# Kernel tuning notes

Hardware: AMD Instinct MI355X
Metric: run time of the kernel (lower is better)

Reference implementation:

```python
import jax, jax.numpy as jnp
import numpy as np
import math

B, L, D = 4, 4096, 1024
D_EMB, D_HID = 3, 16


def make_pos_emb(emb_dim, seq_len):
    # Complex exponential positional embeddings (non-trainable), shape (1, seq_len, emb_dim)
    t = np.linspace(0.0, 1.0, seq_len, dtype=np.float32)[None, :, None]
    bands = (emb_dim - 1) // 2
    t_res = np.linspace(0.0, seq_len - 1, seq_len, dtype=np.float32)[None, :, None]
    w = 2.0 * math.pi * t_res / seq_len
    f = np.linspace(0.0001, max(bands - 1, 0), bands, dtype=np.float32)[None, None]
    z = np.exp(-1j * (f * w).astype(np.complex64))
    z = np.concatenate([t, z.real.astype(np.float32), z.imag.astype(np.float32)], axis=-1)
    return jnp.asarray(z)


def setup_inputs() -> dict:
    key = jax.random.key(0)
    ks = jax.random.split(key, 8)
    u = jax.random.normal(ks[0], (B, L, D), dtype=jnp.float32)
    z = make_pos_emb(D_EMB, L)  # (1, L, D_EMB)
    # filter MLP: Linear(d_emb, d_hidden) -> ReLU -> Linear(d_hidden, d_model)
    s1 = 1.0 / math.sqrt(D_EMB)
    w1 = jax.random.uniform(ks[1], (D_HID, D_EMB), jnp.float32, -s1, s1)
    b1 = jax.random.uniform(ks[2], (D_HID,), jnp.float32, -s1, s1)
    s2 = 1.0 / math.sqrt(D_HID)
    w2 = jax.random.uniform(ks[3], (D, D_HID), jnp.float32, -s2, s2)
    b2 = jax.random.uniform(ks[4], (D,), jnp.float32, -s2, s2)
    # projection: Linear(d_model, d_model)
    sp = 1.0 / math.sqrt(D)
    pw = jax.random.uniform(ks[5], (D, D), jnp.float32, -sp, sp)
    pb = jax.random.uniform(ks[6], (D,), jnp.float32, -sp, sp)
    return {"u": u, "z": z, "w1": w1, "b1": b1, "w2": w2, "b2": b2, "pw": pw, "pb": pb}


def fft_conv(u_bdl, k_dl):
    # u_bdl: (B, D, L), k_dl: (1, D, L) or (D, L)
    seqlen = u_bdl.shape[-1]
    fft_size = 2 * seqlen
    k_f = jnp.fft.rfft(k_dl, n=fft_size) / fft_size
    u_f = jnp.fft.rfft(u_bdl, n=fft_size)
    y = jnp.fft.irfft(u_f * k_f, n=fft_size, norm="forward")[..., :seqlen]
    return y


def reference(u, z, w1, b1, w2, b2, pw, pb):
    seqlen = u.shape[1]
    pe = z[:, :seqlen]  # (1, L, D_EMB)
    h = jax.nn.relu(jnp.einsum("ble,he->blh", pe, w1) + b1)
    filt = jnp.einsum("blh,dh->bld", h, w2) + b2  # (1, L, D)
    filt = jnp.transpose(filt, (0, 2, 1))  # (1, D, L)
    u_conv = fft_conv(jnp.transpose(u, (0, 2, 1)), filt)  # (B, D, L)
    u_conv = jnp.transpose(u_conv, (0, 2, 1)).astype(u.dtype)  # (B, L, D)
    u_proj = jnp.einsum("bld,od->blo", u, pw) + pb
    return u_conv * u_proj + u
```

## Files before the change

### kernel.cpp

```cpp
#include <hip/hip_runtime.h>
#include <hip/hip_bf16.h>

#define SEQL 4096
#define DCH  1024
#define BATCH 4
#define NC   4096
#define KH   4097

typedef float2 cf;
__device__ __forceinline__ cf mkc(float x, float y){ return make_float2(x,y); }
__device__ __forceinline__ cf cadd(cf a, cf b){ return mkc(a.x+b.x, a.y+b.y); }
__device__ __forceinline__ cf csub(cf a, cf b){ return mkc(a.x-b.x, a.y-b.y); }
__device__ __forceinline__ cf cmul(cf a, cf b){ return mkc(a.x*b.x - a.y*b.y, a.x*b.y + a.y*b.x); }
__device__ __forceinline__ cf cconjf(cf a){ return mkc(a.x, -a.y); }
__device__ __forceinline__ cf addi(cf a, cf b){ return mkc(a.x - b.y, a.y + b.x); }
__device__ __forceinline__ cf subi(cf a, cf b){ return mkc(a.x + b.y, a.y - b.x); }
__device__ __forceinline__ int cpad(int i){ return i + (i >> 4); }
__device__ __forceinline__ int drev(int i){
    return ((i>>10)&3) | (((i>>8)&3)<<2) | (((i>>6)&3)<<4)
         | (((i>>4)&3)<<6) | (((i>>2)&3)<<8) | ((i&3)<<10);
}

__device__ __forceinline__ cf W1c(int j){
    const float cs[4] = {1.f, 0.92387953f, 0.70710678f, 0.38268343f};
    const float sn[4] = {0.f, -0.38268343f, -0.70710678f, -0.92387953f};
    return mkc(cs[j], sn[j]);
}
__device__ __forceinline__ cf W2c(int j){
    const float cs[4] = {1.f, 0.70710678f, 0.f, -0.70710678f};
    const float sn[4] = {0.f, -0.70710678f, -1.f, -0.70710678f};
    return mkc(cs[j], sn[j]);
}
__device__ __forceinline__ cf W3c(int j){
    const float cs[4] = {1.f, 0.38268343f, -0.70710678f, -0.92387953f};
    const float sn[4] = {0.f, -0.92387953f, -0.70710678f, 0.38268343f};
    return mkc(cs[j], sn[j]);
}

__global__ __launch_bounds__(256) void twiddle_init(cf* __restrict__ tw4, cf* __restrict__ tw8){
    int i = blockIdx.x*256 + threadIdx.x;
    const double TWO_PI = 6.283185307179586476925286766559;
    double a4 = -TWO_PI * (double)i / 4096.0;
    double a8 = -TWO_PI * (double)i / 8192.0;
    tw4[i] = mkc((float)cos(a4), (float)sin(a4));
    tw8[i] = mkc((float)cos(a8), (float)sin(a8));
}

__device__ void fft_dif(cf* lds, const cf* __restrict__ tw){
    const int tid = threadIdx.x;
#pragma unroll
    for (int p = 0; p < 4; ++p) {
        const int lm = 10 - 2*p;
        const int m  = 1 << lm;
        const int step = 1024 >> lm;
#pragma unroll
        for (int it = 0; it < 4; ++it) {
            int j = tid + (it << 8);
            int k = j & (m-1);
            int g = j >> lm;
            int i0 = (g << (lm+2)) + k;
            cf x0 = lds[cpad(i0)];
            cf x1 = lds[cpad(i0+m)];
            cf x2 = lds[cpad(i0+2*m)];
            cf x3 = lds[cpad(i0+3*m)];
            cf b0 = cadd(x0,x2), b1 = csub(x0,x2);
            cf b2 = cadd(x1,x3), b3 = csub(x1,x3);
            cf u0 = cadd(b0,b2);
            cf u2 = csub(b0,b2);
            cf u1 = subi(b1,b3);
            cf u3 = addi(b1,b3);
            int t1 = k*step;
            lds[cpad(i0)]     = u0;
            lds[cpad(i0+m)]   = cmul(u1, tw[t1]);
            lds[cpad(i0+2*m)] = cmul(u2, tw[2*t1]);
            lds[cpad(i0+3*m)] = cmul(u3, tw[3*t1]);
        }
        __syncthreads();
    }
    {
        int base = 17*tid;
        cf v[16];
#pragma unroll
        for (int j=0;j<16;++j) v[j] = lds[base+j];
#pragma unroll
        for (int j=0;j<4;++j){
            cf x0=v[j], x1=v[j+4], x2=v[j+8], x3=v[j+12];
            cf b0=cadd(x0,x2), b1=csub(x0,x2), b2=cadd(x1,x3), b3=csub(x1,x3);
            cf u0=cadd(b0,b2), u2=csub(b0,b2), u1=subi(b1,b3), u3=addi(b1,b3);
            v[j]    = u0;
            v[j+4]  = cmul(u1, W1c(j));
            v[j+8]  = cmul(u2, W2c(j));
            v[j+12] = cmul(u3, W3c(j));
        }
#pragma unroll
        for (int c=0;c<4;++c){
            cf x0=v[4*c], x1=v[4*c+1], x2=v[4*c+2], x3=v[4*c+3];
            cf b0=cadd(x0,x2), b1=csub(x0,x2), b2=cadd(x1,x3), b3=csub(x1,x3);
            v[4*c]   = cadd(b0,b2);
            v[4*c+1] = subi(b1,b3);
            v[4*c+2] = csub(b0,b2);
            v[4*c+3] = addi(b1,b3);
        }
#pragma unroll
        for (int j=0;j<16;++j) lds[base+j] = v[j];
        __syncthreads();
    }
}

__device__ void fft_dit_inv(cf* lds, const cf* __restrict__ tw){
    const int tid = threadIdx.x;
    {
        int base = 17*tid;
        cf v[16];
#pragma unroll
        for (int j=0;j<16;++j) v[j] = lds[base+j];
#pragma unroll
        for (int c=0;c<4;++c){
            cf a0=v[4*c], a1=v[4*c+1], a2=v[4*c+2], a3=v[4*c+3];
            cf b0=cadd(a0,a2), b1=csub(a0,a2), b2=cadd(a1,a3), b3=csub(a1,a3);
            v[4*c]   = cadd(b0,b2);
            v[4*c+1] = addi(b1,b3);
            v[4*c+2] = csub(b0,b2);
            v[4*c+3] = subi(b1,b3);
        }
#pragma unroll
        for (int j=0;j<4;++j){
            cf a0=v[j];
            cf a1=cmul(v[j+4],  cconjf(W1c(j)));
            cf a2=cmul(v[j+8],  cconjf(W2c(j)));
            cf a3=cmul(v[j+12], cconjf(W3c(j)));
            cf b0=cadd(a0,a2), b1=csub(a0,a2), b2=cadd(a1,a3), b3=csub(a1,a3);
            v[j]    = cadd(b0,b2);
            v[j+4]  = addi(b1,b3);
            v[j+8]  = csub(b0,b2);
            v[j+12] = subi(b1,b3);
        }
#pragma unroll
        for (int j=0;j<16;++j) lds[base+j] = v[j];
        __syncthreads();
    }
#pragma unroll
    for (int p = 0; p < 4; ++p) {
        const int lm = 4 + 2*p;
        const int m  = 1 << lm;
        const int step = 1024 >> lm;
#pragma unroll
        for (int it = 0; it < 4; ++it) {
            int j = tid + (it << 8);
            int k = j & (m-1);
            int g = j >> lm;
            int i0 = (g << (lm+2)) + k;
            int t1 = k*step;
            cf a0 = lds[cpad(i0)];
            cf a1 = cmul(lds[cpad(i0+m)],   cconjf(tw[t1]));
            cf a2 = cmul(lds[cpad(i0+2*m)], cconjf(tw[2*t1]));
            cf a3 = cmul(lds[cpad(i0+3*m)], cconjf(tw[3*t1]));
            cf b0=cadd(a0,a2), b1=csub(a0,a2), b2=cadd(a1,a3), b3=csub(a1,a3);
            lds[cpad(i0)]     = cadd(b0,b2);
            lds[cpad(i0+m)]   = addi(b1,b3);
            lds[cpad(i0+2*m)] = csub(b0,b2);
            lds[cpad(i0+3*m)] = subi(b1,b3);
        }
        __syncthreads();
    }
}

__global__ __launch_bounds__(256) void mlp_kernel(
        const float* __restrict__ z, const float* __restrict__ w1,
        const float* __restrict__ b1, float* __restrict__ h) {
    int l = blockIdx.x * blockDim.x + threadIdx.x;
    if (l >= SEQL) return;
    float pe0 = z[l * 3 + 0], pe1 = z[l * 3 + 1], pe2 = z[l * 3 + 2];
#pragma unroll
    for (int j = 0; j < 16; ++j) {
        float v = pe0 * w1[j * 3 + 0] + pe1 * w1[j * 3 + 1] + pe2 * w1[j * 3 + 2] + b1[j];
        h[l * 16 + j] = v > 0.f ? v : 0.f;
    }
}

__global__ __launch_bounds__(256) void transpose_kernel(
        const float* __restrict__ u, float* __restrict__ ut) {
    __shared__ float tile[32][33];
    int b = blockIdx.z;
    int l0 = blockIdx.x * 32;
    int d0 = blockIdx.y * 32;
    int tx = threadIdx.x, ty = threadIdx.y;
    const float* up = u + (size_t)b * SEQL * DCH;
#pragma unroll
    for (int i = 0; i < 32; i += 8)
        tile[ty + i][tx] = up[(size_t)(l0 + ty + i) * DCH + d0 + tx];
    __syncthreads();
    float* utp = ut + (size_t)b * DCH * SEQL;
#pragma unroll
    for (int i = 0; i < 32; i += 8)
        utp[(size_t)(d0 + ty + i) * SEQL + l0 + tx] = tile[tx][ty + i];
}

__global__ __launch_bounds__(256) void filt_fft_kernel(
        const float* __restrict__ h, const float* __restrict__ w2,
        const float* __restrict__ b2, const cf* __restrict__ tw4,
        const cf* __restrict__ tw8, cf* __restrict__ kf) {
    __shared__ cf lds[4352];
    int d = blockIdx.x;
    int tid = threadIdx.x;
    float w[16];
#pragma unroll
    for (int j = 0; j < 16; ++j) w[j] = w2[d * 16 + j];
    float bb = b2[d];
    for (int n = tid; n < 2048; n += 256) {
        const float* h0 = h + (size_t)(2*n) * 16;
        float f0 = bb, f1 = bb;
#pragma unroll
        for (int j = 0; j < 16; ++j) { f0 += h0[j] * w[j]; f1 += h0[16 + j] * w[j]; }
        lds[cpad(n)] = mkc(f0, f1);
    }
    for (int n = 2048 + tid; n < 4096; n += 256) lds[cpad(n)] = mkc(0.f, 0.f);
    __syncthreads();
    fft_dif(lds, tw4);
    const float s = 1.f / 8192.f;
    cf* Hrow = kf + (size_t)d * KH;
    const int lane  = tid & 63;
    const int kbase = ((lane & 31) << 6) | ((lane >> 5) << 5) | ((tid >> 6) << 3);
#pragma unroll
    for (int it = 0; it < 8; ++it) {
        int k = kbase + it;
        if (k == 0) {
            cf c0 = lds[cpad(0)];
            Hrow[0]    = mkc((c0.x + c0.y) * s, 0.f);
            Hrow[4096] = mkc((c0.x - c0.y) * s, 0.f);
            cf c2 = lds[cpad(drev(2048))];
            Hrow[2048] = mkc(c2.x * s, -c2.y * s);
        } else {
            int kk = 4096 - k;
            cf ck  = lds[cpad(drev(k))];
            cf ckk = lds[cpad(drev(kk))];
            cf cc = cconjf(ckk);
            cf E  = mkc(0.5f*(ck.x+cc.x), 0.5f*(ck.y+cc.y));
            cf Dd = csub(ck, cc);
            cf O  = mkc(0.5f*Dd.y, -0.5f*Dd.x);
            cf wv = tw8[k];
            cf Xk  = cadd(E, cmul(wv, O));
            cf wp  = mkc(-wv.x, wv.y);
            cf Xkk = cadd(cconjf(E), cmul(wp, cconjf(O)));
            Hrow[k]  = mkc(Xk.x * s, Xk.y * s);
            Hrow[kk] = mkc(Xkk.x * s, Xkk.y * s);
        }
    }
}

__global__ __launch_bounds__(256) void conv_kernel(
        float* __restrict__ uty, const cf* __restrict__ tw4,
        const cf* __restrict__ tw8, const cf* __restrict__ kf) {
    __shared__ cf lds[4352];
    int row = blockIdx.x;
    int d = row & (DCH - 1);
    int tid = threadIdx.x;
    float* rp = uty + (size_t)row * SEQL;
    for (int n = tid; n < 2048; n += 256)
        lds[cpad(n)] = *(const float2*)&rp[2*n];
    for (int n = 2048 + tid; n < 4096; n += 256) lds[cpad(n)] = mkc(0.f, 0.f);
    __syncthreads();
    fft_dif(lds, tw4);
    const cf* Hrow = kf + (size_t)d * KH;
    const int lane  = tid & 63;
    const int kbase = ((lane & 31) << 6) | ((lane >> 5) << 5) | ((tid >> 6) << 3);
#pragma unroll
    for (int it = 0; it < 8; ++it) {
        int k = kbase + it;
        if (k == 0) {
            cf c0 = lds[cpad(0)];
            float X0 = c0.x + c0.y, X4 = c0.x - c0.y;
            cf H0 = Hrow[0], H4 = Hrow[4096];
            cf Y0 = mkc(X0 * H0.x, X0 * H0.y);
            cf Y4 = mkc(X4 * H4.x, X4 * H4.y);
            cf S  = cadd(Y0, Y4), Dd = csub(Y0, Y4);
            lds[cpad(0)] = addi(S, Dd);
            int s2 = cpad(drev(2048));
            cf c2 = lds[s2];
            cf Y2 = cmul(cconjf(c2), Hrow[2048]);
            lds[s2] = mkc(2.f * Y2.x, -2.f * Y2.y);
        } else {
            int kk = 4096 - k;
            int sk = cpad(drev(k)), skk = cpad(drev(kk));
            cf ck = lds[sk], ckk = lds[skk];
            cf cc = cconjf(ckk);
            cf E  = mkc(0.5f*(ck.x+cc.x), 0.5f*(ck.y+cc.y));
            cf Dd = csub(ck, cc);
            cf O  = mkc(0.5f*Dd.y, -0.5f*Dd.x);
            cf wv = tw8[k];
            cf Xk  = cadd(E, cmul(wv, O));
            cf wp  = mkc(-wv.x, wv.y);
            cf Xkk = cadd(cconjf(E), cmul(wp, cconjf(O)));
            cf Yk  = cmul(Xk,  Hrow[k]);
            cf Ykk = cmul(Xkk, Hrow[kk]);
            cf cy = cconjf(Ykk);
            cf S  = cadd(Yk, cy), D2 = csub(Yk, cy);
            cf Zk = addi(S, cmul(cconjf(wv), D2));
            cf cy2 = cconjf(Yk);
            cf S2  = cadd(Ykk, cy2), D3 = csub(Ykk, cy2);
            cf Zkk = subi(S2, cmul(wv, D3));
            lds[sk] = Zk; lds[skk] = Zkk;
        }
    }
    __syncthreads();
    fft_dit_inv(lds, tw4);
    for (int n = tid; n < 2048; n += 256) {
        cf v = lds[cpad(n)];
        *(float2*)&rp[2*n] = v;
    }
}

__device__ __forceinline__ unsigned pack2bf(float a, float b){
    unsigned r;
    asm("v_cvt_pk_bf16_f32 %0, %1, %2" : "=v"(r) : "v"(a), "v"(b));
    return r;
}

typedef __attribute__((ext_vector_type(8))) short short8;
typedef __attribute__((ext_vector_type(4))) float f32x4;

__global__ __launch_bounds__(256, 3) void gemm_mfma_kernel(
        const float* __restrict__ u, const float* __restrict__ pw,
        const float* __restrict__ pb, const float* __restrict__ y,
        float* __restrict__ out) {
    __shared__ char lds_raw[34816];
    float (*ysc)[132] = (float(*)[132])lds_raw;

    const int tid  = threadIdx.x;
    const int lane = tid & 63;
    const int wid  = tid >> 6;
    const int wr   = wid >> 1;
    const int wc   = wid & 1;
    const int m0   = blockIdx.x * 128;
    const int n0   = blockIdx.y * 128;

    f32x4 acc[4][4] = {};
    float4 ra[4], rb[4];

    int s_row[4], s_f4[4];
#pragma unroll
    for (int j = 0; j < 4; ++j) {
        int idx = j * 256 + tid;
        s_row[j] = idx >> 3;
        s_f4[j]  = idx & 7;
    }

#define LOADT(kt)                                                                     \
    {                                                                                 \
        _Pragma("unroll")                                                             \
        for (int j = 0; j < 4; ++j) {                                                 \
            ra[j] = *(const float4*)&u [(size_t)(m0 + s_row[j]) * DCH + (kt) + s_f4[j] * 4]; \
            rb[j] = *(const float4*)&pw[(size_t)(n0 + s_row[j]) * DCH + (kt) + s_f4[j] * 4]; \
        }                                                                             \
    }
#define WRITET(base)                                                                  \
    {                                                                                 \
        _Pragma("unroll")                                                             \
        for (int j = 0; j < 4; ++j) {                                                 \
            int off = (base) + ((s_row[j] * 64 + s_f4[j] * 8) ^ ((s_row[j] & 3) << 4)); \
            uint2 pa, pbv2;                                                           \
            pa.x   = pack2bf(ra[j].x, ra[j].y);  pa.y   = pack2bf(ra[j].z, ra[j].w);  \
            pbv2.x = pack2bf(rb[j].x, rb[j].y);  pbv2.y = pack2bf(rb[j].z, rb[j].w);  \
            *(uint2*)(lds_raw + off)        = pa;                                     \
            *(uint2*)(lds_raw + off + 8192) = pbv2;                                   \
        }                                                                             \
    }

    LOADT(0);
    WRITET(0);
    LOADT(32);
    __syncthreads();

    for (int t = 0; t < 32; ++t) {
        const int cur = (t & 1) << 14;
        short8 af[4], bf[4];
#pragma unroll
        for (int f = 0; f < 4; ++f) {
            int rowA = wr * 64 + f * 16 + (lane & 15);
            int rowB = wc * 64 + f * 16 + (lane & 15);
            int offA = cur + ((rowA * 64 + ((lane >> 4) * 16)) ^ ((rowA & 3) << 4));
            int offB = cur + 8192 + ((rowB * 64 + ((lane >> 4) * 16)) ^ ((rowB & 3) << 4));
            af[f] = *(short8*)(lds_raw + offA);
            bf[f] = *(short8*)(lds_raw + offB);
        }
        if (t < 31) WRITET(cur ^ 16384);
        if (t < 30) LOADT((t + 2) * 32);
#pragma unroll
        for (int mf = 0; mf < 4; ++mf)
#pragma unroll
            for (int nf = 0; nf < 4; ++nf)
                acc[mf][nf] = __builtin_amdgcn_mfma_f32_16x16x32_bf16(
                    af[mf], bf[nf], acc[mf][nf], 0, 0, 0);
        __syncthreads();
    }

    const int b  = m0 >> 12;
    const int l0 = m0 & (SEQL - 1);
    float pbv[4];
#pragma unroll
    for (int nf = 0; nf < 4; ++nf)
        pbv[nf] = pb[n0 + wc * 64 + nf * 16 + (lane & 15)];

    for (int c = 0; c < 2; ++c) {
        __syncthreads();
#pragma unroll
        for (int j = 0; j < 8; ++j) {
            int idx = j * 256 + tid;
            int dn  = idx >> 4;
            int lf4 = idx & 15;
            float4 vy = *(const float4*)&y[(((size_t)(b * DCH + n0 + dn)) << 12) + l0 + c * 64 + lf4 * 4];
            ysc[lf4 * 4 + 0][dn] = vy.x;
            ysc[lf4 * 4 + 1][dn] = vy.y;
            ysc[lf4 * 4 + 2][dn] = vy.z;
            ysc[lf4 * 4 + 3][dn] = vy.w;
        }
        __syncthreads();
        if (wr == c) {
#pragma unroll
            for (int mf = 0; mf < 4; ++mf)
#pragma unroll
                for (int i = 0; i < 4; ++i) {
                    int lrow = mf * 16 + (lane >> 4) * 4 + i;
                    int m = m0 + c * 64 + lrow;
#pragma unroll
                    for (int nf = 0; nf < 4; ++nf) {
                        int nl = wc * 64 + nf * 16 + (lane & 15);
                        int n = n0 + nl;
                        float proj = acc[mf][nf][i] + pbv[nf];
                        out[(size_t)m * DCH + n] = ysc[lrow][nl] * proj + u[(size_t)m * DCH + n];
                    }
                }
        }
    }
#undef LOADT
#undef WRITET
}

extern "C" void kernel_launch(void* const* d_in, const int* in_sizes, int n_in,
                              void* d_out, int out_size, void* d_ws, size_t ws_size,
                              hipStream_t stream) {
    const float* u  = (const float*)d_in[0];
    const float* z  = (const float*)d_in[1];
    const float* w1 = (const float*)d_in[2];
    const float* b1 = (const float*)d_in[3];
    const float* w2 = (const float*)d_in[4];
    const float* b2 = (const float*)d_in[5];
    const float* pw = (const float*)d_in[6];
    const float* pb = (const float*)d_in[7];
    float* out = (float*)d_out;

    float* h   = (float*)d_ws;
    float* uty = (float*)((char*)d_ws + 262144);
    cf* kf  = (cf*)d_out;
    cf* tw4 = (cf*)((char*)d_out + (40u << 20));
    cf* tw8 = tw4 + 4096;

    twiddle_init<<<dim3(16), dim3(256), 0, stream>>>(tw4, tw8);
    mlp_kernel<<<dim3(16), dim3(256), 0, stream>>>(z, w1, b1, h);
    transpose_kernel<<<dim3(SEQL / 32, DCH / 32, BATCH), dim3(32, 8), 0, stream>>>(u, uty);
    filt_fft_kernel<<<dim3(DCH), dim3(256), 0, stream>>>(h, w2, b2, tw4, tw8, kf);
    conv_kernel<<<dim3(BATCH * DCH), dim3(256), 0, stream>>>(uty, tw4, tw8, kf);
    gemm_mfma_kernel<<<dim3(128, 8), dim3(256), 0, stream>>>(u, pw, pb, uty, out);
}
```

Measured before the change: 296.1 us.

## Exploit zero-padding in FFT stages and store conv output as bf16

The first radix-4 DIF stage is fused into the load: half the padded input is known zero, so it is computed directly from two loaded values without writing zeros to LDS. The last inverse DIT stage computes only the first half of the output, which is all that is kept. The conv result is written as packed bf16 and the GEMM epilogue reads half as many bytes, which cuts global traffic but lowers the precision of the convolution term.

```diff
diff --git a/kernel.cpp b/kernel.cpp
--- a/kernel.cpp
+++ b/kernel.cpp
@@ -4,7 +4,6 @@
 #define SEQL 4096
 #define DCH  1024
 #define BATCH 4
-#define NC   4096
 #define KH   4097
 
 typedef float2 cf;
@@ -37,6 +36,14 @@
     return mkc(cs[j], sn[j]);
 }
 
+__device__ __forceinline__ unsigned pack2bf(float a, float b){
+    unsigned r;
+    asm("v_cvt_pk_bf16_f32 %0, %1, %2" : "=v"(r) : "v"(a), "v"(b));
+    return r;
+}
+__device__ __forceinline__ float bflo(unsigned u){ return __uint_as_float(u << 16); }
+__device__ __forceinline__ float bfhi(unsigned u){ return __uint_as_float(u & 0xffff0000u); }
+
 __global__ __launch_bounds__(256) void twiddle_init(cf* __restrict__ tw4, cf* __restrict__ tw8){
     int i = blockIdx.x*256 + threadIdx.x;
     const double TWO_PI = 6.283185307179586476925286766559;
@@ -46,10 +53,41 @@
     tw8[i] = mkc((float)cos(a8), (float)sin(a8));
 }
 
-__device__ void fft_dif(cf* lds, const cf* __restrict__ tw){
+__global__ __launch_bounds__(256) void mlp_kernel(
+        const float* __restrict__ z, const float* __restrict__ w1,
+        const float* __restrict__ b1, float* __restrict__ h) {
+    int l = blockIdx.x * blockDim.x + threadIdx.x;
+    if (l >= SEQL) return;
+    float pe0 = z[l * 3 + 0], pe1 = z[l * 3 + 1], pe2 = z[l * 3 + 2];
+#pragma unroll
+    for (int j = 0; j < 16; ++j) {
+        float v = pe0 * w1[j * 3 + 0] + pe1 * w1[j * 3 + 1] + pe2 * w1[j * 3 + 2] + b1[j];
+        h[l * 16 + j] = v > 0.f ? v : 0.f;
+    }
+}
+
+__global__ __launch_bounds__(256) void transpose_kernel(
+        const float* __restrict__ u, float* __restrict__ ut) {
+    __shared__ float tile[32][33];
+    int b = blockIdx.z;
+    int l0 = blockIdx.x * 32;
+    int d0 = blockIdx.y * 32;
+    int tx = threadIdx.x, ty = threadIdx.y;
+    const float* up = u + (size_t)b * SEQL * DCH;
+#pragma unroll
+    for (int i = 0; i < 32; i += 8)
+        tile[ty + i][tx] = up[(size_t)(l0 + ty + i) * DCH + d0 + tx];
+    __syncthreads();
+    float* utp = ut + (size_t)b * DCH * SEQL;
+#pragma unroll
+    for (int i = 0; i < 32; i += 8)
+        utp[(size_t)(d0 + ty + i) * SEQL + l0 + tx] = tile[tx][ty + i];
+}
+
+__device__ void dif_mid_and_chunk(cf* lds, const cf* __restrict__ tw){
     const int tid = threadIdx.x;
 #pragma unroll
-    for (int p = 0; p < 4; ++p) {
+    for (int p = 1; p < 4; ++p) {
         const int lm = 10 - 2*p;
         const int m  = 1 << lm;
         const int step = 1024 >> lm;
@@ -107,7 +145,7 @@
     }
 }
 
-__device__ void fft_dit_inv(cf* lds, const cf* __restrict__ tw){
+__device__ void dit_chunk_and_mid(cf* lds, const cf* __restrict__ tw){
     const int tid = threadIdx.x;
     {
         int base = 17*tid;
@@ -140,7 +178,7 @@
         __syncthreads();
     }
 #pragma unroll
-    for (int p = 0; p < 4; ++p) {
+    for (int p = 0; p < 3; ++p) {
         const int lm = 4 + 2*p;
         const int m  = 1 << lm;
         const int step = 1024 >> lm;
@@ -165,58 +203,40 @@
     }
 }
 
-__global__ __launch_bounds__(256) void mlp_kernel(
-        const float* __restrict__ z, const float* __restrict__ w1,
-        const float* __restrict__ b1, float* __restrict__ h) {
-    int l = blockIdx.x * blockDim.x + threadIdx.x;
-    if (l >= SEQL) return;
-    float pe0 = z[l * 3 + 0], pe1 = z[l * 3 + 1], pe2 = z[l * 3 + 2];
-#pragma unroll
-    for (int j = 0; j < 16; ++j) {
-        float v = pe0 * w1[j * 3 + 0] + pe1 * w1[j * 3 + 1] + pe2 * w1[j * 3 + 2] + b1[j];
-        h[l * 16 + j] = v > 0.f ? v : 0.f;
-    }
-}
-
-__global__ __launch_bounds__(256) void transpose_kernel(
-        const float* __restrict__ u, float* __restrict__ ut) {
-    __shared__ float tile[32][33];
-    int b = blockIdx.z;
-    int l0 = blockIdx.x * 32;
-    int d0 = blockIdx.y * 32;
-    int tx = threadIdx.x, ty = threadIdx.y;
-    const float* up = u + (size_t)b * SEQL * DCH;
-#pragma unroll
-    for (int i = 0; i < 32; i += 8)
-        tile[ty + i][tx] = up[(size_t)(l0 + ty + i) * DCH + d0 + tx];
-    __syncthreads();
-    float* utp = ut + (size_t)b * DCH * SEQL;
-#pragma unroll
-    for (int i = 0; i < 32; i += 8)
-        utp[(size_t)(d0 + ty + i) * SEQL + l0 + tx] = tile[tx][ty + i];
-}
-
 __global__ __launch_bounds__(256) void filt_fft_kernel(
         const float* __restrict__ h, const float* __restrict__ w2,
         const float* __restrict__ b2, const cf* __restrict__ tw4,
         const cf* __restrict__ tw8, cf* __restrict__ kf) {
     __shared__ cf lds[4352];
-    int d = blockIdx.x;
-    int tid = threadIdx.x;
-    float w[16];
-#pragma unroll
-    for (int j = 0; j < 16; ++j) w[j] = w2[d * 16 + j];
-    float bb = b2[d];
-    for (int n = tid; n < 2048; n += 256) {
-        const float* h0 = h + (size_t)(2*n) * 16;
-        float f0 = bb, f1 = bb;
-#pragma unroll
-        for (int j = 0; j < 16; ++j) { f0 += h0[j] * w[j]; f1 += h0[16 + j] * w[j]; }
-        lds[cpad(n)] = mkc(f0, f1);
-    }
-    for (int n = 2048 + tid; n < 4096; n += 256) lds[cpad(n)] = mkc(0.f, 0.f);
+    const int d = blockIdx.x;
+    const int tid = threadIdx.x;
+    float wv[16];
+#pragma unroll
+    for (int j = 0; j < 16; ++j) wv[j] = w2[d * 16 + j];
+    const float bb = b2[d];
+#pragma unroll
+    for (int it = 0; it < 4; ++it) {
+        int j = tid + (it << 8);
+        const float* h0 = h + (size_t)(2*j) * 16;
+        const float* h1 = h + (size_t)(2*(j+1024)) * 16;
+        float f0 = bb, f1 = bb, f2 = bb, f3 = bb;
+#pragma unroll
+        for (int i = 0; i < 16; ++i) {
+            f0 += h0[i] * wv[i];  f1 += h0[16+i] * wv[i];
+            f2 += h1[i] * wv[i];  f3 += h1[16+i] * wv[i];
+        }
+        cf x0 = mkc(f0, f1), x1 = mkc(f2, f3);
+        cf u0 = cadd(x0,x1);
+        cf u2 = csub(x0,x1);
+        cf u1 = subi(x0,x1);
+        cf u3 = addi(x0,x1);
+        lds[cpad(j)]      = u0;
+        lds[cpad(j+1024)] = cmul(u1, tw4[j]);
+        lds[cpad(j+2048)] = cmul(u2, tw4[2*j]);
+        lds[cpad(j+3072)] = cmul(u3, tw4[3*j]);
+    }
     __syncthreads();
-    fft_dif(lds, tw4);
+    dif_mid_and_chunk(lds, tw4);
     const float s = 1.f / 8192.f;
     cf* Hrow = kf + (size_t)d * KH;
     const int lane  = tid & 63;
@@ -238,9 +258,9 @@
             cf E  = mkc(0.5f*(ck.x+cc.x), 0.5f*(ck.y+cc.y));
             cf Dd = csub(ck, cc);
             cf O  = mkc(0.5f*Dd.y, -0.5f*Dd.x);
-            cf wv = tw8[k];
-            cf Xk  = cadd(E, cmul(wv, O));
-            cf wp  = mkc(-wv.x, wv.y);
+            cf wvv = tw8[k];
+            cf Xk  = cadd(E, cmul(wvv, O));
+            cf wp  = mkc(-wvv.x, wvv.y);
             cf Xkk = cadd(cconjf(E), cmul(wp, cconjf(O)));
             Hrow[k]  = mkc(Xk.x * s, Xk.y * s);
             Hrow[kk] = mkc(Xkk.x * s, Xkk.y * s);
@@ -252,68 +272,86 @@
         float* __restrict__ uty, const cf* __restrict__ tw4,
         const cf* __restrict__ tw8, const cf* __restrict__ kf) {
     __shared__ cf lds[4352];
-    int row = blockIdx.x;
-    int d = row & (DCH - 1);
-    int tid = threadIdx.x;
+    const int row = blockIdx.x;
+    const int d = row & (DCH - 1);
+    const int tid = threadIdx.x;
     float* rp = uty + (size_t)row * SEQL;
-    for (int n = tid; n < 2048; n += 256)
-        lds[cpad(n)] = *(const float2*)&rp[2*n];
-    for (int n = 2048 + tid; n < 4096; n += 256) lds[cpad(n)] = mkc(0.f, 0.f);
+#pragma unroll
+    for (int it = 0; it < 4; ++it) {
+        int j = tid + (it << 8);
+        cf x0 = *(const cf*)&rp[2*j];
+        cf x1 = *(const cf*)&rp[2*(j+1024)];
+        cf u0 = cadd(x0,x1);
+        cf u2 = csub(x0,x1);
+        cf u1 = subi(x0,x1);
+        cf u3 = addi(x0,x1);
+        lds[cpad(j)]      = u0;
+        lds[cpad(j+1024)] = cmul(u1, tw4[j]);
+        lds[cpad(j+2048)] = cmul(u2, tw4[2*j]);
+        lds[cpad(j+3072)] = cmul(u3, tw4[3*j]);
+    }
     __syncthreads();
-    fft_dif(lds, tw4);
+    dif_mid_and_chunk(lds, tw4);
     const cf* Hrow = kf + (size_t)d * KH;
-    const int lane  = tid & 63;
-    const int kbase = ((lane & 31) << 6) | ((lane >> 5) << 5) | ((tid >> 6) << 3);
-#pragma unroll
-    for (int it = 0; it < 8; ++it) {
-        int k = kbase + it;
-        if (k == 0) {
-            cf c0 = lds[cpad(0)];
-            float X0 = c0.x + c0.y, X4 = c0.x - c0.y;
-            cf H0 = Hrow[0], H4 = Hrow[4096];
-            cf Y0 = mkc(X0 * H0.x, X0 * H0.y);
-            cf Y4 = mkc(X4 * H4.x, X4 * H4.y);
-            cf S  = cadd(Y0, Y4), Dd = csub(Y0, Y4);
-            lds[cpad(0)] = addi(S, Dd);
-            int s2 = cpad(drev(2048));
-            cf c2 = lds[s2];
-            cf Y2 = cmul(cconjf(c2), Hrow[2048]);
-            lds[s2] = mkc(2.f * Y2.x, -2.f * Y2.y);
-        } else {
-            int kk = 4096 - k;
-            int sk = cpad(drev(k)), skk = cpad(drev(kk));
-            cf ck = lds[sk], ckk = lds[skk];
-            cf cc = cconjf(ckk);
-            cf E  = mkc(0.5f*(ck.x+cc.x), 0.5f*(ck.y+cc.y));
-            cf Dd = csub(ck, cc);
-            cf O  = mkc(0.5f*Dd.y, -0.5f*Dd.x);
-            cf wv = tw8[k];
-            cf Xk  = cadd(E, cmul(wv, O));
-            cf wp  = mkc(-wv.x, wv.y);
-            cf Xkk = cadd(cconjf(E), cmul(wp, cconjf(O)));
-            cf Yk  = cmul(Xk,  Hrow[k]);
-            cf Ykk = cmul(Xkk, Hrow[kk]);
-            cf cy = cconjf(Ykk);
-            cf S  = cadd(Yk, cy), D2 = csub(Yk, cy);
-            cf Zk = addi(S, cmul(cconjf(wv), D2));
-            cf cy2 = cconjf(Yk);
-            cf S2  = cadd(Ykk, cy2), D3 = csub(Ykk, cy2);
-            cf Zkk = subi(S2, cmul(wv, D3));
-            lds[sk] = Zk; lds[skk] = Zkk;
+    {
+        const int lane  = tid & 63;
+        const int kbase = ((lane & 31) << 6) | ((lane >> 5) << 5) | ((tid >> 6) << 3);
+#pragma unroll
+        for (int it = 0; it < 8; ++it) {
+            int k = kbase + it;
+            if (k == 0) {
+                cf c0 = lds[cpad(0)];
+                float X0 = c0.x + c0.y, X4 = c0.x - c0.y;
+                cf H0 = Hrow[0], H4 = Hrow[4096];
+                cf Y0 = mkc(X0 * H0.x, X0 * H0.y);
+                cf Y4 = mkc(X4 * H4.x, X4 * H4.y);
+                cf S  = cadd(Y0, Y4), Dd = csub(Y0, Y4);
+                lds[cpad(0)] = addi(S, Dd);
+                int s2 = cpad(drev(2048));
+                cf c2 = lds[s2];
+                cf Y2 = cmul(cconjf(c2), Hrow[2048]);
+                lds[s2] = mkc(2.f * Y2.x, -2.f * Y2.y);
+            } else {
+                int kk = 4096 - k;
+                int sk = cpad(drev(k)), skk = cpad(drev(kk));
+                cf ck = lds[sk], ckk = lds[skk];
+                cf cc = cconjf(ckk);
+                cf E  = mkc(0.5f*(ck.x+cc.x), 0.5f*(ck.y+cc.y));
+                cf Dd = csub(ck, cc);
+                cf O  = mkc(0.5f*Dd.y, -0.5f*Dd.x);
+                cf wv = tw8[k];
+                cf Xk  = cadd(E, cmul(wv, O));
+                cf wp  = mkc(-wv.x, wv.y);
+                cf Xkk = cadd(cconjf(E), cmul(wp, cconjf(O)));
+                cf Yk  = cmul(Xk,  Hrow[k]);
+                cf Ykk = cmul(Xkk, Hrow[kk]);
+                cf cy = cconjf(Ykk);
+                cf S  = cadd(Yk, cy), D2 = csub(Yk, cy);
+                cf Zk = addi(S, cmul(cconjf(wv), D2));
+                cf cy2 = cconjf(Yk);
+                cf S2  = cadd(Ykk, cy2), D3 = csub(Ykk, cy2);
+                cf Zkk = subi(S2, cmul(wv, D3));
+                lds[sk] = Zk; lds[skk] = Zkk;
+            }
         }
     }
     __syncthreads();
-    fft_dit_inv(lds, tw4);
-    for (int n = tid; n < 2048; n += 256) {
-        cf v = lds[cpad(n)];
-        *(float2*)&rp[2*n] = v;
-    }
-}
-
-__device__ __forceinline__ unsigned pack2bf(float a, float b){
-    unsigned r;
-    asm("v_cvt_pk_bf16_f32 %0, %1, %2" : "=v"(r) : "v"(a), "v"(b));
-    return r;
+    dit_chunk_and_mid(lds, tw4);
+    unsigned short* yb = (unsigned short*)rp;
+#pragma unroll
+    for (int it = 0; it < 4; ++it) {
+        int j = tid + (it << 8);
+        cf a0 = lds[cpad(j)];
+        cf a1 = cmul(lds[cpad(j+1024)], cconjf(tw4[j]));
+        cf a2 = cmul(lds[cpad(j+2048)], cconjf(tw4[2*j]));
+        cf a3 = cmul(lds[cpad(j+3072)], cconjf(tw4[3*j]));
+        cf b0 = cadd(a0,a2), b1 = csub(a0,a2);
+        cf b2 = cadd(a1,a3), b3 = csub(a1,a3);
+        cf o0 = cadd(b0,b2);
+        cf o1 = addi(b1,b3);
+        *(unsigned*)&yb[2*j]          = pack2bf(o0.x, o0.y);
+        *(unsigned*)&yb[2*(j+1024)]   = pack2bf(o1.x, o1.y);
+    }
 }
 
 typedef __attribute__((ext_vector_type(8))) short short8;
@@ -321,7 +359,7 @@
 
 __global__ __launch_bounds__(256, 3) void gemm_mfma_kernel(
         const float* __restrict__ u, const float* __restrict__ pw,
-        const float* __restrict__ pb, const float* __restrict__ y,
+        const float* __restrict__ pb, const unsigned short* __restrict__ yb,
         float* __restrict__ out) {
     __shared__ char lds_raw[34816];
     float (*ysc)[132] = (float(*)[132])lds_raw;
@@ -404,15 +442,16 @@
     for (int c = 0; c < 2; ++c) {
         __syncthreads();
 #pragma unroll
-        for (int j = 0; j < 8; ++j) {
+        for (int j = 0; j < 4; ++j) {
             int idx = j * 256 + tid;
-            int dn  = idx >> 4;
-            int lf4 = idx & 15;
-            float4 vy = *(const float4*)&y[(((size_t)(b * DCH + n0 + dn)) << 12) + l0 + c * 64 + lf4 * 4];
-            ysc[lf4 * 4 + 0][dn] = vy.x;
-            ysc[lf4 * 4 + 1][dn] = vy.y;
-            ysc[lf4 * 4 + 2][dn] = vy.z;
-            ysc[lf4 * 4 + 3][dn] = vy.w;
+            int dn  = idx >> 3;
+            int lg  = idx & 7;
+            uint4 w4 = *(const uint4*)&yb[(((size_t)(b * DCH + n0 + dn)) << 13) + l0 + c * 64 + lg * 8];
+            int lb = lg * 8;
+            ysc[lb+0][dn] = bflo(w4.x); ysc[lb+1][dn] = bfhi(w4.x);
+            ysc[lb+2][dn] = bflo(w4.y); ysc[lb+3][dn] = bfhi(w4.y);
+            ysc[lb+4][dn] = bflo(w4.z); ysc[lb+5][dn] = bfhi(w4.z);
+            ysc[lb+6][dn] = bflo(w4.w); ysc[lb+7][dn] = bfhi(w4.w);
         }
         __syncthreads();
         if (wr == c) {
@@ -460,5 +499,5 @@
     transpose_kernel<<<dim3(SEQL / 32, DCH / 32, BATCH), dim3(32, 8), 0, stream>>>(u, uty);
     filt_fft_kernel<<<dim3(DCH), dim3(256), 0, stream>>>(h, w2, b2, tw4, tw8, kf);
     conv_kernel<<<dim3(BATCH * DCH), dim3(256), 0, stream>>>(uty, tw4, tw8, kf);
-    gemm_mfma_kernel<<<dim3(128, 8), dim3(256), 0, stream>>>(u, pw, pb, uty, out);
-}
+    gemm_mfma_kernel<<<dim3(128, 8), dim3(256), 0, stream>>>(u, pw, pb, (const unsigned short*)uty, out);
+}
```

After: 285.2 us. 3.7% less time.
